# Kernel optimization log

Hardware: AMD Instinct MI355X
Metric: run time of the kernel (lower is better)

The kernel has to match this reference:

```python
import jax, jax.numpy as jnp
import numpy as np
import math

B, T, D = 2, 2048, 512      # batch, n_tp, input_dim
DM, H = 64, 16              # per-head d_model, nhead


def setup_inputs() -> dict:
    key = jax.random.key(0)
    ks = jax.random.split(key, 12)
    s = 0.02
    return {
        "data": jax.random.normal(ks[0], (B, T, D), jnp.float32),
        "mask": jax.random.uniform(ks[1], (B, T, D), jnp.float32),
        "wq": jax.random.normal(ks[2], (D, DM * H), jnp.float32) * s,
        "bq": jnp.zeros((DM * H,), jnp.float32),
        "wk": jax.random.normal(ks[3], (D, DM * H), jnp.float32) * s,
        "bk": jnp.zeros((DM * H,), jnp.float32),
        "wv": jax.random.normal(ks[4], (D, DM * H), jnp.float32) * s,
        "bv": jnp.zeros((DM * H,), jnp.float32),
        "wo": jax.random.normal(ks[5], (DM * H, D), jnp.float32) * s,
        "bo": jnp.zeros((D,), jnp.float32),
    }


def reference(data, mask, wq, bq, wk, bk, wv, bv, wo, bo):
    b, t, d = data.shape
    # NOTE: torch code splits proj as (d_model, nhead): head index is fastest-varying
    def split_heads(x):  # [b,t,DM*H] -> [b,H,t,DM]
        return x.reshape(b, t, DM, H).transpose(0, 3, 1, 2)

    q = split_heads(data @ wq + bq)
    k = split_heads(data @ wk + bk)
    v = split_heads(data @ wv + bv)

    scores = jnp.einsum("bhqd,bhkd->bhqk", q, k) / math.sqrt(DM)
    # padded key positions: rows of mask that sum to exactly 0
    pad = (jnp.sum(mask, axis=-1) == 0.0)  # [b, t] (key axis)
    scores = jnp.where(pad[:, None, None, :], -1e9, scores)
    attn = jax.nn.softmax(scores, axis=-1)  # dropout = identity (eval mode)
    out = jnp.einsum("bhqk,bhkd->bhqd", attn, v)
    # merge as (nhead, d_model) — matches torch permute(0,2,1,3).reshape
    out = out.transpose(0, 2, 1, 3).reshape(b, t, H * DM)
    return out @ wo + bo
```

## Files before the change

### kernel.cpp

```cpp
#include <hip/hip_runtime.h>
#include <hip/hip_bf16.h>

#define B_  2
#define T_  2048
#define D_  512
#define DM_ 64
#define H_  16
#define NQ_ (DM_*H_)
#define NP_ (T_/128)

typedef __bf16 bf16x8 __attribute__((ext_vector_type(8)));
typedef __bf16 bf16x4 __attribute__((ext_vector_type(4)));
typedef float  f32x4  __attribute__((ext_vector_type(4)));
typedef unsigned int u32;

static __device__ __forceinline__ __bf16 bfc(float x) { return (__bf16)x; }
static __device__ __forceinline__ unsigned short f2bf(float x) {
    __bf16 b = (__bf16)x;
    unsigned short u;
    __builtin_memcpy(&u, &b, 2);
    return u;
}
static __device__ __forceinline__ u32 pack2bf(float a, float b) {
    return (u32)f2bf(a) | ((u32)f2bf(b) << 16);
}

#if __has_builtin(__builtin_amdgcn_exp2f)
static __device__ __forceinline__ float EXP2(float x) { return __builtin_amdgcn_exp2f(x); }
#else
static __device__ __forceinline__ float EXP2(float x) {
    float r; asm("v_exp_f32 %0, %1\ns_nop 0" : "=v"(r) : "v"(x)); return r;
}
#endif

#define GLOAD16(gp, lp) \
    __builtin_amdgcn_global_load_lds((const __attribute__((address_space(1))) u32*)(gp), \
                                     (__attribute__((address_space(3))) u32*)(lp), 16, 0, 0)

__global__ __launch_bounds__(256)
void prep_kernel(const float* __restrict__ mask, float* __restrict__ padb,
                 const float* __restrict__ data, unsigned short* __restrict__ dataB,
                 const float* __restrict__ wq, const float* __restrict__ wk,
                 const float* __restrict__ wv, unsigned short* __restrict__ btall,
                 const float* __restrict__ wo, unsigned short* __restrict__ wot)
{
    __shared__ float t[32][33];
    const int bid = blockIdx.x;
    const int tid = threadIdx.x;
    if (bid < 1024) {
        const int row  = bid * 4 + (tid >> 6);
        const int lane = tid & 63;
        const float* p = mask + (size_t)row * D_;
        float4 a = *(const float4*)&p[lane * 8];
        float4 b = *(const float4*)&p[lane * 8 + 4];
        float s = a.x + a.y + a.z + a.w + b.x + b.y + b.z + b.w;
#pragma unroll
        for (int off = 32; off; off >>= 1) s += __shfl_down(s, off);
        if (lane == 0) padb[row] = (s == 0.0f) ? -1e9f : 0.0f;
    } else if (bid < 2048) {
        int i = ((bid - 1024) * 256 + tid) * 8;
        float4 a = *(const float4*)&data[i];
        float4 b = *(const float4*)&data[i + 4];
        bf16x8 u = {bfc(a.x), bfc(a.y), bfc(a.z), bfc(a.w),
                    bfc(b.x), bfc(b.y), bfc(b.z), bfc(b.w)};
        *(bf16x8*)&dataB[i] = u;
    } else if (bid < 3584) {
        const int idx = bid - 2048;
        const int z = idx >> 9, rem = idx & 511;
        const int c0 = (rem & 31) * 32, r0 = (rem >> 5) * 32;
        const float* in = (z == 0) ? wq : (z == 1) ? wk : wv;
        unsigned short* out = btall + (size_t)z * NQ_ * D_;
        const int tx = tid & 31, ty = tid >> 5;
#pragma unroll
        for (int i = 0; i < 4; ++i)
            t[ty * 4 + i][tx] = in[(size_t)(r0 + ty * 4 + i) * NQ_ + c0 + tx];
        __syncthreads();
#pragma unroll
        for (int i = 0; i < 4; ++i)
            out[(size_t)(c0 + ty * 4 + i) * D_ + r0 + tx] = f2bf(t[tx][ty * 4 + i]);
    } else {
        const int idx = bid - 3584;
        const int c0 = (idx & 15) * 32, r0 = (idx >> 4) * 32;
        const int tx = tid & 31, ty = tid >> 5;
#pragma unroll
        for (int i = 0; i < 4; ++i)
            t[ty * 4 + i][tx] = wo[(size_t)(r0 + ty * 4 + i) * D_ + c0 + tx];
        __syncthreads();
#pragma unroll
        for (int i = 0; i < 4; ++i)
            wot[(size_t)(c0 + ty * 4 + i) * NQ_ + r0 + tx] = f2bf(t[tx][ty * 4 + i]);
    }
}

__global__ __launch_bounds__(256)
void mgemm_qkv_kernel(const unsigned short* __restrict__ A,
                      const unsigned short* __restrict__ BtAll,
                      const float* __restrict__ bq, const float* __restrict__ bk,
                      const float* __restrict__ bv,
                      unsigned short* __restrict__ Qh, unsigned short* __restrict__ Kh,
                      unsigned short* __restrict__ Vt, float alpha_q)
{
    const int K = D_;
    __shared__ __align__(16) unsigned short Al[2][128 * 64];
    __shared__ __align__(16) unsigned short Bl[2][128 * 64];

    const int tid = threadIdx.x;
    const int w  = tid >> 6, l = tid & 63;
    const int lo = l & 15,  g = l >> 4;
    const int wri = w >> 1, wci = w & 1;
    const int m0 = blockIdx.y * 128, n0 = blockIdx.x * 128;
    const int lrow = l >> 3;
    const int lslot = (l & 7) ^ lrow;

    f32x4 acc[4][4] = {};
    const int nk = K >> 6;

#pragma unroll
    for (int p = 0; p < 4; ++p) {
        int br = w * 32 + p * 8;
        GLOAD16(A     + (size_t)(m0 + br + lrow) * K + lslot * 8, (char*)Al[0] + br * 128);
        GLOAD16(BtAll + (size_t)(n0 + br + lrow) * K + lslot * 8, (char*)Bl[0] + br * 128);
    }
    __syncthreads();

    for (int t = 0; t < nk; ++t) {
        const int cur = t & 1;
        if (t + 1 < nk) {
            const int k0 = (t + 1) << 6;
#pragma unroll
            for (int p = 0; p < 4; ++p) {
                int br = w * 32 + p * 8;
                GLOAD16(A     + (size_t)(m0 + br + lrow) * K + k0 + lslot * 8,
                        (char*)Al[cur ^ 1] + br * 128);
                GLOAD16(BtAll + (size_t)(n0 + br + lrow) * K + k0 + lslot * 8,
                        (char*)Bl[cur ^ 1] + br * 128);
            }
        }
#pragma unroll
        for (int kk = 0; kk < 2; ++kk) {
            bf16x8 af[4], bfr[4];
#pragma unroll
            for (int i = 0; i < 4; ++i) {
                int row = wri * 64 + i * 16 + lo;
                af[i] = *(const bf16x8*)&Al[cur][row * 64 + ((((kk << 2) + g) ^ (row & 7)) << 3)];
                int col = wci * 64 + i * 16 + lo;
                bfr[i] = *(const bf16x8*)&Bl[cur][col * 64 + ((((kk << 2) + g) ^ (col & 7)) << 3)];
            }
#pragma unroll
            for (int i = 0; i < 4; ++i)
#pragma unroll
                for (int j = 0; j < 4; ++j)
                    acc[i][j] = __builtin_amdgcn_mfma_f32_16x16x32_bf16(af[i], bfr[j], acc[i][j], 0, 0, 0);
        }
        __syncthreads();
    }

    const int seg = n0 >> 10;
    const int n0l = n0 & 1023;
    const float* bias = (seg == 0) ? bq : (seg == 1) ? bk : bv;
    const float alpha = (seg == 0) ? alpha_q : 1.0f;
    unsigned short* o16 = (seg == 0) ? Qh : (seg == 1) ? Kh : Vt;

    const int mb = m0 + wri * 64 + g * 4;
    float bb[4];
#pragma unroll
    for (int j = 0; j < 4; ++j) bb[j] = bias[n0l + wci * 64 + j * 16 + lo];
    const int head = lo;
    const int dmb  = (n0l >> 4) + wci * 4;
    if (seg < 2) {
#pragma unroll
        for (int i = 0; i < 4; ++i)
#pragma unroll
            for (int jj = 0; jj < 4; ++jj) {
                int m = mb + i * 16 + jj;
                int t = m & (T_ - 1), bidx = m >> 11;
                bf16x4 u = {bfc((acc[i][0][jj] + bb[0]) * alpha),
                            bfc((acc[i][1][jj] + bb[1]) * alpha),
                            bfc((acc[i][2][jj] + bb[2]) * alpha),
                            bfc((acc[i][3][jj] + bb[3]) * alpha)};
                *(bf16x4*)&o16[(((size_t)(bidx * H_ + head)) * T_ + t) * DM_ + dmb] = u;
            }
    } else {
#pragma unroll
        for (int i = 0; i < 4; ++i)
#pragma unroll
            for (int j = 0; j < 4; ++j) {
                int m = mb + i * 16;
                int t = m & (T_ - 1), bidx = m >> 11;
                bf16x4 u = {bfc(acc[i][j][0] + bb[j]), bfc(acc[i][j][1] + bb[j]),
                            bfc(acc[i][j][2] + bb[j]), bfc(acc[i][j][3] + bb[j])};
                *(bf16x4*)&o16[((size_t)(bidx * H_ + head) * DM_ + dmb + j) * T_ + t] = u;
            }
    }
}

__global__ __launch_bounds__(256)
void mgemm_out_kernel(const unsigned short* __restrict__ A,
                      const unsigned short* __restrict__ Bt,
                      const float* __restrict__ bias, float* __restrict__ out,
                      int M, int N, int K)
{
    __shared__ __align__(16) unsigned short Al[2][64 * 64];
    __shared__ __align__(16) unsigned short Bl[2][128 * 64];

    const int tid = threadIdx.x;
    const int w  = tid >> 6, l = tid & 63;
    const int lo = l & 15,  g = l >> 4;
    const int wri = w >> 1, wci = w & 1;
    const int m0 = blockIdx.y * 64, n0 = blockIdx.x * 128;
    const int lrow = l >> 3;
    const int lslot = (l & 7) ^ lrow;

    f32x4 acc[2][4] = {};
    const int nk = K >> 6;

#pragma unroll
    for (int p = 0; p < 2; ++p) {
        int br = w * 16 + p * 8;
        GLOAD16(A + (size_t)(m0 + br + lrow) * K + lslot * 8, (char*)Al[0] + br * 128);
    }
#pragma unroll
    for (int p = 0; p < 4; ++p) {
        int br = w * 32 + p * 8;
        GLOAD16(Bt + (size_t)(n0 + br + lrow) * K + lslot * 8, (char*)Bl[0] + br * 128);
    }
    __syncthreads();

    for (int t = 0; t < nk; ++t) {
        const int cur = t & 1;
        if (t + 1 < nk) {
            const int k0 = (t + 1) << 6;
#pragma unroll
            for (int p = 0; p < 2; ++p) {
                int br = w * 16 + p * 8;
                GLOAD16(A + (size_t)(m0 + br + lrow) * K + k0 + lslot * 8,
                        (char*)Al[cur ^ 1] + br * 128);
            }
#pragma unroll
            for (int p = 0; p < 4; ++p) {
                int br = w * 32 + p * 8;
                GLOAD16(Bt + (size_t)(n0 + br + lrow) * K + k0 + lslot * 8,
                        (char*)Bl[cur ^ 1] + br * 128);
            }
        }
#pragma unroll
        for (int kk = 0; kk < 2; ++kk) {
            bf16x8 af[2], bfr[4];
#pragma unroll
            for (int i = 0; i < 2; ++i) {
                int row = wri * 32 + i * 16 + lo;
                af[i] = *(const bf16x8*)&Al[cur][row * 64 + ((((kk << 2) + g) ^ (row & 7)) << 3)];
            }
#pragma unroll
            for (int j = 0; j < 4; ++j) {
                int col = wci * 64 + j * 16 + lo;
                bfr[j] = *(const bf16x8*)&Bl[cur][col * 64 + ((((kk << 2) + g) ^ (col & 7)) << 3)];
            }
#pragma unroll
            for (int i = 0; i < 2; ++i)
#pragma unroll
                for (int j = 0; j < 4; ++j)
                    acc[i][j] = __builtin_amdgcn_mfma_f32_16x16x32_bf16(af[i], bfr[j], acc[i][j], 0, 0, 0);
        }
        __syncthreads();
    }

    const int mb = m0 + wri * 32 + g * 4;
#pragma unroll
    for (int j = 0; j < 4; ++j) {
        int n = n0 + wci * 64 + j * 16 + lo;
        float bb = bias[n];
#pragma unroll
        for (int i = 0; i < 2; ++i)
#pragma unroll
            for (int jj = 0; jj < 4; ++jj) {
                int m = mb + i * 16 + jj;
                out[(size_t)m * N + n] = acc[i][j][jj] + bb;
            }
    }
}

__global__ __launch_bounds__(256, 2)
void attn_kernel(const unsigned short* __restrict__ Qh,
                 const unsigned short* __restrict__ Kh,
                 const unsigned short* __restrict__ Vt,
                 const float* __restrict__ padb,
                 unsigned short* __restrict__ ctx)
{
    __shared__ __align__(16) unsigned short Ks[4][64 * 64];
    __shared__ __align__(16) unsigned short Vs[4][64 * 64];
    __shared__ __align__(16) float pbs[T_];

    const int tid  = threadIdx.x;
    const int w    = tid >> 6;
    const int l    = tid & 63;
    const int lo16 = l & 15;
    const int g    = l >> 4;
    const int lrow = l >> 3;
    const int lslot = (l & 7) ^ lrow;

    const int f   = blockIdx.x;
    const int s   = f >> 3;
    const int bh  = (f & 7) * 4 + (s >> 4);
    const int q0  = (s & 15) * 128;
    const int bb  = bh >> 4;
    const int hh  = bh & 15;

    bf16x8 qf[2][2];
#pragma unroll
    for (int qt = 0; qt < 2; ++qt) {
        const unsigned short* Qp =
            Qh + ((size_t)bh * T_ + q0 + w * 32 + qt * 16 + lo16) * DM_ + g * 8;
        qf[qt][0] = *(const bf16x8*)(Qp);
        qf[qt][1] = *(const bf16x8*)(Qp + 32);
    }

    const unsigned short* kgp =
        Kh + (size_t)bh * T_ * DM_ + (size_t)(w * 16 + lrow) * DM_ + lslot * 8;
    const unsigned short* vgp =
        Vt + (size_t)bh * DM_ * T_ + (size_t)(w * 16 + lrow) * T_ + lslot * 8;

    {
        const float* src = padb + bb * T_ + tid * 8;
        *(float4*)&pbs[tid * 8]     = *(const float4*)(src);
        *(float4*)&pbs[tid * 8 + 4] = *(const float4*)(src + 4);
    }

    GLOAD16(kgp,                (char*)Ks[0] + (w * 16) * 128);
    GLOAD16(kgp + 8 * DM_,      (char*)Ks[0] + (w * 16 + 8) * 128);
    GLOAD16(kgp + 64 * DM_,     (char*)Ks[1] + (w * 16) * 128);
    GLOAD16(kgp + 72 * DM_,     (char*)Ks[1] + (w * 16 + 8) * 128);
    GLOAD16(vgp,                (char*)Vs[0] + (w * 16) * 128);
    GLOAD16(vgp + 8 * T_,       (char*)Vs[0] + (w * 16 + 8) * 128);
    GLOAD16(vgp + 64,           (char*)Vs[1] + (w * 16) * 128);
    GLOAD16(vgp + 8 * T_ + 64,  (char*)Vs[1] + (w * 16 + 8) * 128);
    kgp += 128 * DM_;
    vgp += 128;
    __syncthreads();

    f32x4 oa[2][4] = {};
    f32x4 ls4[2] = {};

    char* KrA = (char*)Ks[0]; char* KrB = (char*)Ks[1];
    char* KwA = (char*)Ks[2]; char* KwB = (char*)Ks[3];
    char* VrA = (char*)Vs[0]; char* VrB = (char*)Vs[1];
    char* VwA = (char*)Vs[2]; char* VwB = (char*)Vs[3];

    auto process = [&](const char* Kt, const char* Vc, int pboff) {
        f32x4 sa[2][4];
#pragma unroll
        for (int nt = 0; nt < 4; ++nt) {
            f32x4 pb4 = *(const f32x4*)&pbs[pboff + nt * 16 + g * 4];
            sa[0][nt] = pb4;
            sa[1][nt] = pb4;
        }
        __builtin_amdgcn_s_setprio(1);
#pragma unroll
        for (int ks = 0; ks < 2; ++ks) {
#pragma unroll
            for (int nt = 0; nt < 4; ++nt) {
                int row = nt * 16 + lo16;
                int off = (row * 128 + ks * 64 + g * 16) ^ ((row & 7) << 4);
                bf16x8 kf = *(const bf16x8*)(Kt + off);
#pragma unroll
                for (int qt = 0; qt < 2; ++qt)
                    sa[qt][nt] = __builtin_amdgcn_mfma_f32_16x16x32_bf16(kf, qf[qt][ks], sa[qt][nt], 0, 0, 0);
            }
        }
        __builtin_amdgcn_s_setprio(0);

        u32 pw[2][4][2];
#pragma unroll
        for (int qt = 0; qt < 2; ++qt)
#pragma unroll
            for (int nt = 0; nt < 4; ++nt) {
                float e0 = EXP2(sa[qt][nt][0]);
                float e1 = EXP2(sa[qt][nt][1]);
                float e2 = EXP2(sa[qt][nt][2]);
                float e3 = EXP2(sa[qt][nt][3]);
                ls4[qt] += (f32x4){e0, e1, e2, e3};
                pw[qt][nt][0] = pack2bf(e0, e1);
                pw[qt][nt][1] = pack2bf(e2, e3);
            }
        bf16x8 pf[2][2];
#pragma unroll
        for (int qt = 0; qt < 2; ++qt)
#pragma unroll
            for (int ks = 0; ks < 2; ++ks) {
                uint4 uu;
                uu.x = pw[qt][2 * ks][0];
                uu.y = pw[qt][2 * ks][1];
                uu.z = pw[qt][2 * ks + 1][0];
                uu.w = pw[qt][2 * ks + 1][1];
                pf[qt][ks] = *(const bf16x8*)&uu;
            }

        __builtin_amdgcn_s_setprio(1);
#pragma unroll
        for (int ks = 0; ks < 2; ++ks)
#pragma unroll
            for (int nd = 0; nd < 4; ++nd) {
                int row = nd * 16 + lo16;
                int sw = (row & 7) << 4;
                int o0 = (row * 128 + ks * 64 + g * 8) ^ sw;
                int o1 = (row * 128 + ks * 64 + 32 + g * 8) ^ sw;
                uint2 a = *(const uint2*)(Vc + o0);
                uint2 b = *(const uint2*)(Vc + o1);
                uint4 uu; uu.x = a.x; uu.y = a.y; uu.z = b.x; uu.w = b.y;
                bf16x8 vf = *(const bf16x8*)&uu;
#pragma unroll
                for (int qt = 0; qt < 2; ++qt)
                    oa[qt][nd] = __builtin_amdgcn_mfma_f32_16x16x32_bf16(vf, pf[qt][ks], oa[qt][nd], 0, 0, 0);
            }
        __builtin_amdgcn_s_setprio(0);
    };

    for (int p = 0; p < NP_; ++p) {
        if (p + 1 < NP_) {
            GLOAD16(kgp,               KwA + (w * 16) * 128);
            GLOAD16(kgp + 8 * DM_,     KwA + (w * 16 + 8) * 128);
            GLOAD16(kgp + 64 * DM_,    KwB + (w * 16) * 128);
            GLOAD16(kgp + 72 * DM_,    KwB + (w * 16 + 8) * 128);
            GLOAD16(vgp,               VwA + (w * 16) * 128);
            GLOAD16(vgp + 8 * T_,      VwA + (w * 16 + 8) * 128);
            GLOAD16(vgp + 64,          VwB + (w * 16) * 128);
            GLOAD16(vgp + 8 * T_ + 64, VwB + (w * 16 + 8) * 128);
            kgp += 128 * DM_;
            vgp += 128;
        }

        process(KrA, VrA, p * 128);
        process(KrB, VrB, p * 128 + 64);

        __syncthreads();
        { char* t0;
          t0 = KrA; KrA = KwA; KwA = t0;
          t0 = KrB; KrB = KwB; KwB = t0;
          t0 = VrA; VrA = VwA; VwA = t0;
          t0 = VrB; VrB = VwB; VwB = t0; }
    }

#pragma unroll
    for (int qt = 0; qt < 2; ++qt) {
        float lt = (ls4[qt][0] + ls4[qt][1]) + (ls4[qt][2] + ls4[qt][3]);
        lt += __shfl_xor(lt, 16);
        lt += __shfl_xor(lt, 32);
        float linv = 1.0f / lt;
        const size_t crow =
            ((size_t)(bb * T_ + q0 + w * 32 + qt * 16 + lo16)) * NQ_ + hh * DM_;
#pragma unroll
        for (int nd = 0; nd < 4; ++nd) {
            bf16x4 u = {bfc(oa[qt][nd][0] * linv), bfc(oa[qt][nd][1] * linv),
                        bfc(oa[qt][nd][2] * linv), bfc(oa[qt][nd][3] * linv)};
            *(bf16x4*)&ctx[crow + nd * 16 + g * 4] = u;
        }
    }
}

extern "C" void kernel_launch(void* const* d_in, const int* in_sizes, int n_in,
                              void* d_out, int out_size, void* d_ws, size_t ws_size,
                              hipStream_t stream) {
    const float* data = (const float*)d_in[0];
    const float* mask = (const float*)d_in[1];
    const float* wq   = (const float*)d_in[2];
    const float* bq   = (const float*)d_in[3];
    const float* wk   = (const float*)d_in[4];
    const float* bk   = (const float*)d_in[5];
    const float* wv   = (const float*)d_in[6];
    const float* bv   = (const float*)d_in[7];
    const float* wo   = (const float*)d_in[8];
    const float* bo   = (const float*)d_in[9];
    float* out = (float*)d_out;

    char* ws = (char*)d_ws;
    const size_t MB = 1024 * 1024;
    unsigned short* Qh    = (unsigned short*)(ws);
    unsigned short* Kh    = (unsigned short*)(ws +  8 * MB);
    unsigned short* Vt    = (unsigned short*)(ws + 16 * MB);
    unsigned short* CTX   = (unsigned short*)(ws + 24 * MB);
    unsigned short* dataB = (unsigned short*)(ws + 32 * MB);
    unsigned short* BtAll = (unsigned short*)(ws + 36 * MB);
    unsigned short* wot   = (unsigned short*)(ws + 39 * MB);
    float*          padb  = (float*)         (ws + 40 * MB);

    const int M = B_ * T_;
    const float alpha_q = 0.125f * 1.44269504089f;

    prep_kernel<<<4096, 256, 0, stream>>>(mask, padb, data, dataB,
                                          wq, wk, wv, BtAll, wo, wot);

    mgemm_qkv_kernel<<<dim3(3 * NQ_ / 128, M / 128), 256, 0, stream>>>(
        dataB, BtAll, bq, bk, bv, Qh, Kh, Vt, alpha_q);

    attn_kernel<<<512, 256, 0, stream>>>(Qh, Kh, Vt, padb, CTX);

    mgemm_out_kernel<<<dim3(D_ / 128, M / 64), 256, 0, stream>>>(
        CTX, wot, bo, out, M, D_, NQ_);
}
```

Baseline: 105.3 us.

## Permute QKV weight columns to head-major and stage Q/K epilogue through LDS

The weight transpose now writes the Q/K/V weight columns head-major, so each 64-column GEMM tile maps to one whole head. The Q/K epilogue writes its results into swizzled LDS and then issues coalesced 16-byte row stores. Before, it made scattered 8-byte stores across 16 heads. This is meant to cut uncoalesced global writes in the QKV projection, at the cost of an extra LDS round trip and a barrier. The bias indexing and the V transpose store change to match the new column order.

```diff
diff --git a/kernel.cpp b/kernel.cpp
--- a/kernel.cpp
+++ b/kernel.cpp
@@ -76,8 +76,11 @@
             t[ty * 4 + i][tx] = in[(size_t)(r0 + ty * 4 + i) * NQ_ + c0 + tx];
         __syncthreads();
 #pragma unroll
-        for (int i = 0; i < 4; ++i)
-            out[(size_t)(c0 + ty * 4 + i) * D_ + r0 + tx] = f2bf(t[tx][ty * 4 + i]);
+        for (int i = 0; i < 4; ++i) {
+            int c  = c0 + ty * 4 + i;
+            int rp = (c & 15) * 64 + (c >> 4);
+            out[(size_t)rp * D_ + r0 + tx] = f2bf(t[tx][ty * 4 + i]);
+        }
     } else {
         const int idx = bid - 3584;
         const int c0 = (idx & 15) * 32, r0 = (idx >> 4) * 32;
@@ -159,37 +162,49 @@
     const int n0l = n0 & 1023;
     const float* bias = (seg == 0) ? bq : (seg == 1) ? bk : bv;
     const float alpha = (seg == 0) ? alpha_q : 1.0f;
-    unsigned short* o16 = (seg == 0) ? Qh : (seg == 1) ? Kh : Vt;
-
-    const int mb = m0 + wri * 64 + g * 4;
+    const int h = (n0l >> 6) + wci;
+
     float bb[4];
 #pragma unroll
-    for (int j = 0; j < 4; ++j) bb[j] = bias[n0l + wci * 64 + j * 16 + lo];
-    const int head = lo;
-    const int dmb  = (n0l >> 4) + wci * 4;
+    for (int j = 0; j < 4; ++j) bb[j] = bias[(j * 16 + lo) * 16 + h];
+
+    const int mb_l = wri * 64 + g * 4;
     if (seg < 2) {
+        unsigned short* o16 = (seg == 0) ? Qh : Kh;
+        unsigned short* hb = (unsigned short*)Al + wci * (128 * 64);
 #pragma unroll
         for (int i = 0; i < 4; ++i)
 #pragma unroll
             for (int jj = 0; jj < 4; ++jj) {
-                int m = mb + i * 16 + jj;
+                int ml = mb_l + i * 16 + jj;
+#pragma unroll
+                for (int j = 0; j < 4; ++j) {
+                    int dm = j * 16 + lo;
+                    int off = ml * 64 + (((dm >> 3) ^ (ml & 7)) << 3) + (dm & 7);
+                    hb[off] = f2bf((acc[i][j][jj] + bb[j]) * alpha);
+                }
+            }
+        __syncthreads();
+        const int rrow = l >> 3, rch = l & 7;
+#pragma unroll
+        for (int p = 0; p < 8; ++p) {
+            int ml = wri * 64 + p * 8 + rrow;
+            bf16x8 v = *(const bf16x8*)&hb[ml * 64 + (((rch ^ (ml & 7))) << 3)];
+            int m = m0 + ml;
+            int t = m & (T_ - 1), bidx = m >> 11;
+            *(bf16x8*)&o16[(((size_t)(bidx * H_ + h)) * T_ + t) * DM_ + rch * 8] = v;
+        }
+    } else {
+#pragma unroll
+        for (int i = 0; i < 4; ++i)
+#pragma unroll
+            for (int j = 0; j < 4; ++j) {
+                int m = m0 + mb_l + i * 16;
                 int t = m & (T_ - 1), bidx = m >> 11;
-                bf16x4 u = {bfc((acc[i][0][jj] + bb[0]) * alpha),
-                            bfc((acc[i][1][jj] + bb[1]) * alpha),
-                            bfc((acc[i][2][jj] + bb[2]) * alpha),
-                            bfc((acc[i][3][jj] + bb[3]) * alpha)};
-                *(bf16x4*)&o16[(((size_t)(bidx * H_ + head)) * T_ + t) * DM_ + dmb] = u;
-            }
-    } else {
-#pragma unroll
-        for (int i = 0; i < 4; ++i)
-#pragma unroll
-            for (int j = 0; j < 4; ++j) {
-                int m = mb + i * 16;
-                int t = m & (T_ - 1), bidx = m >> 11;
+                int dm = j * 16 + lo;
                 bf16x4 u = {bfc(acc[i][j][0] + bb[j]), bfc(acc[i][j][1] + bb[j]),
                             bfc(acc[i][j][2] + bb[j]), bfc(acc[i][j][3] + bb[j])};
-                *(bf16x4*)&o16[((size_t)(bidx * H_ + head) * DM_ + dmb + j) * T_ + t] = u;
+                *(bf16x4*)&Vt[((size_t)(bidx * H_ + h) * DM_ + dm) * T_ + t] = u;
             }
     }
 }
```

New measurement: 98.82 us. 6.1% less time.
